# Kernel tuning notes

Hardware: AMD Instinct MI355X
Metric: run time of the kernel (lower is better)

Reference implementation:

```python
import jax, jax.numpy as jnp
import numpy as np

# Lorentz hyperboloid with curvature -1 (k = 1): <x,x>_L = -1/k, x0 = time coord.
K_CURV = 1.0
EPS = 1e-8
B, N, D, H = 4, 1024, 1024, 16
HD = D // H  # dim_per_head = 64 (space dims per head)


def _time(space):
    # time coord so the point lies on the hyperboloid
    return jnp.sqrt(jnp.sum(space * space, axis=-1, keepdims=True) + 1.0 / K_CURV)


def _lift(space):
    return jnp.concatenate([_time(space), space], axis=-1)


def _linner(u, v):
    # Minkowski inner product <u,v>_L = -u0 v0 + u_s . v_s
    return jnp.sum(u[..., 1:] * v[..., 1:], axis=-1) - u[..., 0] * v[..., 0]


def _lorentz_layernorm(x, gamma, beta):
    s = x[..., 1:]
    mu = jnp.mean(s, axis=-1, keepdims=True)
    var = jnp.mean((s - mu) ** 2, axis=-1, keepdims=True)
    s = (s - mu) / jnp.sqrt(var + 1e-5) * gamma + beta
    return _lift(s)


def _lorentz_linear(x, W, b):
    # linear on the full Lorentz point -> space part of output, time recomputed
    return _lift(x @ W + b)


def _lresnet(x, y, w):
    # Lorentzian residual: (x + w*y) renormalized back onto the hyperboloid
    z = x + w * y
    denom = jnp.sqrt(jnp.clip(-_linner(z, z), EPS))[..., None]
    return z / (jnp.sqrt(K_CURV) * denom)


def _attention(x, Wq, bq, Wk, bk, Wv, bv, Wo, bo):
    def heads(W, b):
        s = (x @ W + b).reshape(B, N, H, HD).transpose(0, 2, 1, 3)  # [B,H,N,HD]
        return _lift(s)  # per-head Lorentz points [B,H,N,HD+1]

    q, k, v = heads(Wq, bq), heads(Wk, bk), heads(Wv, bv)
    sgn = jnp.concatenate([-jnp.ones((1,), x.dtype), jnp.ones((HD,), x.dtype)])
    # pairwise Minkowski inner products; score = -d_L^2 = 2/k + 2<q,k>_L, scaled
    scores = jnp.einsum('bhqd,bhkd->bhqk', q * sgn, k)
    scores = (2.0 / K_CURV + 2.0 * scores) / np.sqrt(HD).astype(np.float32)
    attn = jax.nn.softmax(scores, axis=-1)
    # Lorentz midpoint aggregation of values
    mid = jnp.einsum('bhqk,bhkd->bhqd', attn, v)
    denom = jnp.sqrt(jnp.clip(-_linner(mid, mid), EPS))[..., None]
    mid = mid / (jnp.sqrt(K_CURV) * denom)  # [B,H,N,HD+1]
    cat = mid.transpose(0, 2, 1, 3).reshape(B, N, H * (HD + 1))  # trans_heads_concat
    return _lift(cat @ Wo + bo)


def reference(x, g1, b1, Wq, bq, Wk, bk, Wv, bv, Wo, bo, g2, b2, Wfc, bfc, Wpj, bpj, w1, w2):
    lx = _lorentz_layernorm(x, g1, b1)
    ax = _attention(lx, Wq, bq, Wk, bk, Wv, bv, Wo, bo)
    x = _lresnet(x, ax, w1)
    h = _lorentz_layernorm(x, g2, b2)
    h = _lorentz_linear(h, Wfc, bfc)                      # [B,N,4D]
    h = _lift(jax.nn.gelu(h[..., 1:], approximate=False))  # LorentzActivation(GELU)
    h = _lorentz_linear(h, Wpj, bpj)                      # [B,N,D]
    return _lresnet(x, h, w2)


def setup_inputs() -> dict:
    key = jax.random.key(0)
    ks = jax.random.split(key, 8)
    sc = 0.02
    f32 = jnp.float32
    xs = jax.random.normal(ks[0], (B, N, D - 1), f32)
    return dict(
        x=_lift(xs),
        g1=jnp.ones((D - 1,), f32), b1=jnp.zeros((D - 1,), f32),
        Wq=sc * jax.random.normal(ks[1], (D, H * HD), f32), bq=jnp.zeros((H * HD,), f32),
        Wk=sc * jax.random.normal(ks[2], (D, H * HD), f32), bk=jnp.zeros((H * HD,), f32),
        Wv=sc * jax.random.normal(ks[3], (D, H * HD), f32), bv=jnp.zeros((H * HD,), f32),
        Wo=sc * jax.random.normal(ks[4], (H * (HD + 1), D - 1), f32), bo=jnp.zeros((D - 1,), f32),
        g2=jnp.ones((D - 1,), f32), b2=jnp.zeros((D - 1,), f32),
        Wfc=sc * jax.random.normal(ks[5], (D, 4 * D - 1), f32), bfc=jnp.zeros((4 * D - 1,), f32),
        Wpj=sc * jax.random.normal(ks[6], (4 * D, D - 1), f32), bpj=jnp.zeros((D - 1,), f32),
        w1=jnp.ones((), f32), w2=jnp.ones((), f32),
    )
```

## Files before the change

### kernel.cpp

```cpp
#include <hip/hip_runtime.h>
#include <math.h>

#define BB 4
#define NN 1024
#define DD 1024
#define HH 16
#define ROWS (BB*NN)

typedef __attribute__((ext_vector_type(8))) short bf16x8;
typedef __attribute__((ext_vector_type(4))) float f32x4;
typedef unsigned short u16;

__device__ __forceinline__ u16 f2bf(float f) {
    union { float f; unsigned u; } v; v.f = f;
    unsigned r = v.u + 0x7fff + ((v.u >> 16) & 1);
    return (u16)(r >> 16);
}
__device__ __forceinline__ float bf2f(u16 u) {
    union { unsigned u; float f; } v; v.u = ((unsigned)u) << 16; return v.f;
}

__device__ __forceinline__ void async16(const void* g, void* l) {
    __builtin_amdgcn_global_load_lds(
        (__attribute__((address_space(1))) void*)(uintptr_t)g,
        (__attribute__((address_space(3))) void*)(uintptr_t)l,
        16, 0, 0);
}

__device__ __forceinline__ float block_reduce_sum(float v, float* sm) {
    #pragma unroll
    for (int o = 32; o > 0; o >>= 1) v += __shfl_down(v, o);
    int lane = threadIdx.x & 63, wid = threadIdx.x >> 6;
    if (lane == 0) sm[wid] = v;
    __syncthreads();
    if (wid == 0) {
        v = (lane < (int)(blockDim.x >> 6)) ? sm[lane] : 0.f;
        #pragma unroll
        for (int o = 2; o > 0; o >>= 1) v += __shfl_down(v, o);
        if (lane == 0) sm[0] = v;
    }
    __syncthreads();
    float r = sm[0];
    __syncthreads();
    return r;
}

__global__ __launch_bounds__(256) void k_pre(
        const float* __restrict__ Wq_, const float* __restrict__ Wk_,
        const float* __restrict__ Wv_, const float* __restrict__ Wo_,
        const float* __restrict__ Wfc_, const float* __restrict__ Wpj_,
        u16* __restrict__ WqkvT, u16* __restrict__ WoT,
        u16* __restrict__ WfcT, u16* __restrict__ WpjT,
        const float* __restrict__ x, const float* __restrict__ g1,
        const float* __restrict__ be1, u16* __restrict__ lnout) {
    __shared__ float t[32][33];
    int bid = blockIdx.x;
    if (bid < 12352) {
        const float* W; u16* out; int K, N, Kpad, Npad, gx;
        if (bid < 1024)      { W = Wq_;  out = WqkvT;            K = 1024; N = 1024; Kpad = 1024; Npad = 1024; gx = 32; }
        else if (bid < 2048) { W = Wk_;  out = WqkvT + 1048576;  K = 1024; N = 1024; Kpad = 1024; Npad = 1024; gx = 32; bid -= 1024; }
        else if (bid < 3072) { W = Wv_;  out = WqkvT + 2097152;  K = 1024; N = 1024; Kpad = 1024; Npad = 1024; gx = 32; bid -= 2048; }
        else if (bid < 4160) { W = Wo_;  out = WoT;              K = 1040; N = 1023; Kpad = 1088; Npad = 1024; gx = 34; bid -= 3072; }
        else if (bid < 8256) { W = Wfc_; out = WfcT;             K = 1024; N = 4095; Kpad = 1024; Npad = 4096; gx = 32; bid -= 4160; }
        else                 { W = Wpj_; out = WpjT;             K = 4096; N = 1023; Kpad = 4096; Npad = 1024; gx = 128; bid -= 8256; }
        int k0 = (bid % gx) * 32, n0 = (bid / gx) * 32;
        int tx = threadIdx.x & 31, ty = threadIdx.x >> 5;
        #pragma unroll
        for (int i = 0; i < 32; i += 8) {
            int k = k0 + ty + i, n = n0 + tx;
            t[ty + i][tx] = (k < K && n < N) ? W[(size_t)k * N + n] : 0.f;
        }
        __syncthreads();
        #pragma unroll
        for (int i = 0; i < 32; i += 8) {
            int n = n0 + ty + i, k = k0 + tx;
            if (n < Npad && k < Kpad) out[(size_t)n * Kpad + k] = f2bf(t[tx][ty + i]);
        }
    } else {
        float* sm = &t[0][0];
        int row = bid - 12352;
        const float* xr = x + (size_t)row * DD;
        u16* orow = lnout + (size_t)row * DD;
        float s = 0.f, ss = 0.f;
        for (int j = threadIdx.x; j < DD - 1; j += blockDim.x) {
            float v = xr[1 + j]; s += v; ss += v * v;
        }
        s = block_reduce_sum(s, sm);
        ss = block_reduce_sum(ss, sm);
        float mu = s / (float)(DD - 1);
        float var = ss / (float)(DD - 1) - mu * mu;
        float rstd = rsqrtf(var + 1e-5f);
        float s2 = 0.f;
        for (int j = threadIdx.x; j < DD - 1; j += blockDim.x) {
            float v = (xr[1 + j] - mu) * rstd * g1[j] + be1[j];
            orow[1 + j] = f2bf(v); s2 += v * v;
        }
        s2 = block_reduce_sum(s2, sm);
        if (threadIdx.x == 0) orow[0] = f2bf(sqrtf(s2 + 1.f));
    }
}

__device__ __forceinline__ void cstore(float* p, float v) { *p = v; }
__device__ __forceinline__ void cstore(u16* p, float v) { *p = f2bf(v); }

template <typename OT>
__global__ __launch_bounds__(256) void k_gemm_mfma(
        const u16* __restrict__ A, const u16* __restrict__ BT,
        const float* __restrict__ bias, int nbias,
        OT* __restrict__ C0, OT* __restrict__ C1,
        int ldc, int ldab, int ksplit, int K) {
    __shared__ __align__(16) u16 As[2][128 * 64];
    __shared__ __align__(16) u16 Bs[2][128 * 64];
    int z = blockIdx.z;
    int kbeg = z ? ksplit : 0;
    int kend = z ? K : ksplit;
    OT* C = z ? C1 : C0;
    const float* bs = z ? nullptr : bias;

    int tid = threadIdx.x;
    int wave = tid >> 6, lane = tid & 63;
    int quad = lane >> 4, m16 = lane & 15;
    int n0 = blockIdx.x * 128, m0 = blockIdx.y * 128;
    int wm = (wave & 1) * 64, wn = (wave >> 1) * 64;

    f32x4 acc[4][4];
    #pragma unroll
    for (int t = 0; t < 4; ++t)
        #pragma unroll
        for (int u = 0; u < 4; ++u) acc[t][u] = (f32x4){0.f, 0.f, 0.f, 0.f};

    int r8 = lane >> 3;
    int cc = (lane & 7) ^ r8;
    int srow = wave * 32 + r8;
    const u16* ag = A  + (size_t)(m0 + srow) * ldab + cc * 8;
    const u16* bg = BT + (size_t)(n0 + srow) * ldab + cc * 8;

    auto stage = [&](int k0, int s) {
        #pragma unroll
        for (int j = 0; j < 4; ++j) {
            async16(ag + (size_t)(j * 8) * ldab + k0, &As[s][(wave * 32 + j * 8) * 64]);
            async16(bg + (size_t)(j * 8) * ldab + k0, &Bs[s][(wave * 32 + j * 8) * 64]);
        }
    };

    int niter = (kend - kbeg) >> 6;
    stage(kbeg, 0);
    for (int it = 0; it < niter; ++it) {
        int cur = it & 1;
        __syncthreads();
        if (it + 1 < niter) stage(kbeg + (it + 1) * 64, cur ^ 1);
        #pragma unroll
        for (int kk = 0; kk < 2; ++kk) {
            bf16x8 af[4], bfr[4];
            #pragma unroll
            for (int t = 0; t < 4; ++t) {
                int slot = (kk * 4 + quad) ^ (m16 & 7);
                af[t] = *(const bf16x8*)&As[cur][(wm + t * 16 + m16) * 64 + slot * 8];
            }
            #pragma unroll
            for (int u = 0; u < 4; ++u) {
                int slot = (kk * 4 + quad) ^ (m16 & 7);
                bfr[u] = *(const bf16x8*)&Bs[cur][(wn + u * 16 + m16) * 64 + slot * 8];
            }
            #pragma unroll
            for (int t = 0; t < 4; ++t)
                #pragma unroll
                for (int u = 0; u < 4; ++u)
                    acc[t][u] = __builtin_amdgcn_mfma_f32_16x16x32_bf16(af[t], bfr[u], acc[t][u], 0, 0, 0);
        }
    }
    #pragma unroll
    for (int u = 0; u < 4; ++u) {
        int col = n0 + wn + u * 16 + m16;
        float bv = (bs != nullptr && col < nbias) ? bs[col] : 0.f;
        #pragma unroll
        for (int t = 0; t < 4; ++t) {
            #pragma unroll
            for (int r = 0; r < 4; ++r) {
                int row = m0 + wm + t * 16 + quad * 4 + r;
                cstore(C + (size_t)row * ldc + col, acc[t][u][r] + bv);
            }
        }
    }
}

__global__ __launch_bounds__(256) void k_build_heads(
        const u16* __restrict__ qkv,
        const float* __restrict__ bq, const float* __restrict__ bk,
        const float* __restrict__ bv,
        u16* __restrict__ Qp, u16* __restrict__ Kp, u16* __restrict__ V2) {
    int wid = threadIdx.x >> 6, lane = threadIdx.x & 63;
    int idx = blockIdx.x * 4 + wid;
    int h = idx & 15, bn = idx >> 4;
    int b = bn >> 10, n = bn & 1023;
    int sec = blockIdx.y;
    const float* bias = (sec == 0) ? bq : (sec == 1) ? bk : bv;
    float v = bf2f(qkv[(size_t)bn * 3072 + sec * 1024 + h * 64 + lane]) + bias[h * 64 + lane];
    float ss = v * v;
    #pragma unroll
    for (int o = 32; o > 0; o >>= 1) ss += __shfl_xor(ss, o);
    float tcomp = sqrtf(ss + 1.f);
    size_t bhn = (size_t)(b * 16 + h) * 1024 + n;
    if (sec == 0) {
        u16* drow = Qp + bhn * 96;
        drow[1 + lane] = f2bf(v);
        if (lane == 0) drow[0] = f2bf(-tcomp);
        if (lane < 31) drow[65 + lane] = 0;
    } else if (sec == 1) {
        u16* drow = Kp + bhn * 104;
        drow[1 + lane] = f2bf(v);
        if (lane == 0) drow[0] = f2bf(tcomp);
        if (lane < 39) drow[65 + lane] = 0;
    } else {
        u16* base = V2 + ((size_t)(b * 16 + h) * 16 + (n >> 6)) * 6144 + (n & 63);
        base[(1 + lane) * 72] = f2bf(v);
        if (lane == 0) base[0] = f2bf(tcomp);
        if (lane >= 49) base[(16 + lane) * 72] = 0;
    }
}

#define AKS 104
#define AVS 72
#define APS 88
#define KTILE_U16 (64 * AKS)
#define VTILE_U16 6144
#define EXPC 0.36067376f
__global__ __launch_bounds__(256) void k_attn_mfma(
        const u16* __restrict__ Qp, const u16* __restrict__ Kp,
        const u16* __restrict__ V2, u16* __restrict__ cat) {
    __shared__ __align__(16) u16 Klds[2][KTILE_U16];
    __shared__ __align__(16) u16 Vlds[2][VTILE_U16];
    __shared__ __align__(16) u16 Plds[4][16 * APS];
    int tid = threadIdx.x;
    int wave = tid >> 6, lane = tid & 63;
    int quad = lane >> 4, m = lane & 15;
    int bid = blockIdx.x;
    int bh = ((bid & 7) << 3) | (bid >> 6);
    int qt = (bid >> 3) & 7;

    const u16* kg = Kp + (size_t)bh * 16 * KTILE_U16;
    const u16* vg = V2 + (size_t)bh * 16 * VTILE_U16;

    bf16x8 aq[2][3];
    #pragma unroll
    for (int g = 0; g < 2; ++g) {
        const u16* qptr = Qp + ((size_t)bh * 1024 + qt * 128 + g * 64 + wave * 16 + m) * 96;
        aq[g][0] = *(const bf16x8*)(qptr + quad * 8);
        aq[g][1] = *(const bf16x8*)(qptr + 32 + quad * 8);
        aq[g][2] = *(const bf16x8*)(qptr + 64 + quad * 8);
    }

    f32x4 O[2][5];
    #pragma unroll
    for (int g = 0; g < 2; ++g)
        #pragma unroll
        for (int i = 0; i < 5; ++i) O[g][i] = (f32x4){0.f, 0.f, 0.f, 0.f};

    auto stage = [&](int kt, int s) {
        const u16* kt_p = kg + kt * KTILE_U16 + lane * 8;
        const u16* vt_p = vg + kt * VTILE_U16 + lane * 8;
        for (int i = wave; i < 25; i += 4) {
            if (i < 13) async16(kt_p + i * 512, &Klds[s][i * 512]);
            else        async16(vt_p + (i - 13) * 512, &Vlds[s][(i - 13) * 512]);
        }
    };

    stage(0, 0);
    for (int kt = 0; kt < 16; ++kt) {
        int cur = kt & 1;
        __syncthreads();
        if (kt < 15) stage(kt + 1, cur ^ 1);
        u16* pw = &Plds[wave][0];
        #pragma unroll
        for (int g = 0; g < 2; ++g) {
            #pragma unroll
            for (int nt = 0; nt < 4; ++nt) {
                f32x4 acc = (f32x4){0.f, 0.f, 0.f, 0.f};
                const u16* kr = &Klds[cur][(nt * 16 + m) * AKS + quad * 8];
                acc = __builtin_amdgcn_mfma_f32_16x16x32_bf16(*(const bf16x8*)(kr),      aq[g][0], acc, 0, 0, 0);
                acc = __builtin_amdgcn_mfma_f32_16x16x32_bf16(*(const bf16x8*)(kr + 32), aq[g][1], acc, 0, 0, 0);
                acc = __builtin_amdgcn_mfma_f32_16x16x32_bf16(*(const bf16x8*)(kr + 64), aq[g][2], acc, 0, 0, 0);
                unsigned pk0, pk1;
                {
                    union { float f; unsigned u; } a0, a1, a2, a3;
                    a0.f = __builtin_amdgcn_exp2f(fmaf(acc[0], EXPC, EXPC));
                    a1.f = __builtin_amdgcn_exp2f(fmaf(acc[1], EXPC, EXPC));
                    a2.f = __builtin_amdgcn_exp2f(fmaf(acc[2], EXPC, EXPC));
                    a3.f = __builtin_amdgcn_exp2f(fmaf(acc[3], EXPC, EXPC));
                    pk0 = ((a0.u + 0x8000u) >> 16) | (((a1.u + 0x8000u) >> 16) << 16);
                    pk1 = ((a2.u + 0x8000u) >> 16) | (((a3.u + 0x8000u) >> 16) << 16);
                }
                uint2 pk; pk.x = pk0; pk.y = pk1;
                *(uint2*)&pw[m * APS + nt * 16 + quad * 4] = pk;
            }
            #pragma unroll
            for (int kc = 0; kc < 2; ++kc) {
                bf16x8 ap = *(const bf16x8*)&Plds[wave][m * APS + kc * 32 + quad * 8];
                #pragma unroll
                for (int vt = 0; vt < 5; ++vt) {
                    bf16x8 bv = *(const bf16x8*)&Vlds[cur][(vt * 16 + m) * AVS + kc * 32 + quad * 8];
                    O[g][vt] = __builtin_amdgcn_mfma_f32_16x16x32_bf16(ap, bv, O[g][vt], 0, 0, 0);
                }
            }
        }
    }
    int b = bh >> 4, h = bh & 15;
    #pragma unroll
    for (int g = 0; g < 2; ++g) {
        #pragma unroll
        for (int r = 0; r < 4; ++r) {
            float part = 0.f;
            #pragma unroll
            for (int vt = 0; vt < 5; ++vt) {
                int c = vt * 16 + m;
                float o = O[g][vt][r];
                part += (c == 0) ? o * o : -o * o;
            }
            part += __shfl_xor(part, 1);
            part += __shfl_xor(part, 2);
            part += __shfl_xor(part, 4);
            part += __shfl_xor(part, 8);
            float rden = rsqrtf(fmaxf(part, 1e-8f));
            int n = qt * 128 + g * 64 + wave * 16 + quad * 4 + r;
            u16* crow = cat + (size_t)(b * 1024 + n) * 1088 + h * 65;
            #pragma unroll
            for (int vt = 0; vt < 5; ++vt) {
                int c = vt * 16 + m;
                if (c < 65) crow[c] = f2bf(O[g][vt][r] * rden);
            }
        }
    }
    if (h == 15) {
        for (int i = tid; i < 128 * 48; i += 256) {
            int rr = i / 48, c = i - rr * 48;
            int n = qt * 128 + rr;
            cat[(size_t)(b * 1024 + n) * 1088 + 1040 + c] = 0;
        }
    }
}

__global__ __launch_bounds__(256) void k_lresnet_ln(
        const float* __restrict__ x, const float* __restrict__ y0,
        const float* __restrict__ y1, const float* __restrict__ wscale,
        const float* __restrict__ g2, const float* __restrict__ be2,
        float* __restrict__ x1, u16* __restrict__ lnout) {
    __shared__ float sm[8];
    int row = blockIdx.x;
    const float* xr = x + (size_t)row * DD;
    const float* ya = y0 + (size_t)row * 1024;
    const float* yb = y1 + (size_t)row * 1024;
    float w = *wscale;
    float zreg[4];
    float sy = 0.f, sz = 0.f, szs = 0.f;
    int cnt = 0;
    for (int j = threadIdx.x; j < DD - 1; j += blockDim.x) {
        float yv = ya[j] + yb[j];
        float zv = xr[1 + j] + w * yv;
        sy += yv * yv; sz += zv * zv; szs += zv;
        zreg[cnt++] = zv;
    }
    sy = block_reduce_sum(sy, sm);
    sz = block_reduce_sum(sz, sm);
    szs = block_reduce_sum(szs, sm);
    float y0t = sqrtf(sy + 1.f);
    float z0 = xr[0] + w * y0t;
    float q = z0 * z0 - sz;
    float rden = rsqrtf(fmaxf(q, 1e-8f));
    float mu = rden * szs / (float)(DD - 1);
    float ex2 = rden * rden * sz / (float)(DD - 1);
    float var = ex2 - mu * mu;
    float rstd = rsqrtf(var + 1e-5f);
    float s2 = 0.f;
    cnt = 0;
    float* x1r = x1 + (size_t)row * DD;
    u16* lr = lnout + (size_t)row * DD;
    for (int j = threadIdx.x; j < DD - 1; j += blockDim.x) {
        float xv = zreg[cnt++] * rden;
        x1r[1 + j] = xv;
        float v = (xv - mu) * rstd * g2[j] + be2[j];
        lr[1 + j] = f2bf(v); s2 += v * v;
    }
    s2 = block_reduce_sum(s2, sm);
    if (threadIdx.x == 0) {
        x1r[0] = z0 * rden;
        lr[0] = f2bf(sqrtf(s2 + 1.f));
    }
}

__global__ __launch_bounds__(256) void k_lresnet(
        const float* __restrict__ x, const float* __restrict__ y0,
        const float* __restrict__ y1, const float* __restrict__ wscale,
        float* __restrict__ out) {
    __shared__ float sm[8];
    int row = blockIdx.x;
    const float* xr = x + (size_t)row * DD;
    const float* ya = y0 + (size_t)row * 1024;
    const float* yb = y1 + (size_t)row * 1024;
    float w = *wscale;
    float zreg[4];
    float sy = 0.f, sz = 0.f;
    int cnt = 0;
    for (int j = threadIdx.x; j < DD - 1; j += blockDim.x) {
        float yv = ya[j] + yb[j];
        float zv = xr[1 + j] + w * yv;
        sy += yv * yv; sz += zv * zv;
        zreg[cnt++] = zv;
    }
    sy = block_reduce_sum(sy, sm);
    sz = block_reduce_sum(sz, sm);
    float y0t = sqrtf(sy + 1.f);
    float z0 = xr[0] + w * y0t;
    float q = z0 * z0 - sz;
    float rden = rsqrtf(fmaxf(q, 1e-8f));
    cnt = 0;
    for (int j = threadIdx.x; j < DD - 1; j += blockDim.x)
        out[(size_t)row * DD + 1 + j] = zreg[cnt++] * rden;
    if (threadIdx.x == 0) out[(size_t)row * DD] = z0 * rden;
}

__global__ __launch_bounds__(256) void k_gelu_lift(
        const u16* __restrict__ hfc, u16* __restrict__ hg) {
    __shared__ float sm[8];
    int row = blockIdx.x;
    const u16* hr = hfc + (size_t)row * 4096;
    u16* gr = hg + (size_t)row * 4096;
    float s2 = 0.f;
    for (int j = threadIdx.x; j < 4095; j += blockDim.x) {
        float v = bf2f(hr[j]);
        float gl = 0.5f * v * (1.f + erff(v * 0.70710678f));
        gr[1 + j] = f2bf(gl); s2 += gl * gl;
    }
    s2 = block_reduce_sum(s2, sm);
    if (threadIdx.x == 0) gr[0] = f2bf(sqrtf(s2 + 1.f));
}

extern "C" void kernel_launch(void* const* d_in, const int* in_sizes, int n_in,
                              void* d_out, int out_size, void* d_ws, size_t ws_size,
                              hipStream_t stream) {
    const float* x   = (const float*)d_in[0];
    const float* g1  = (const float*)d_in[1];
    const float* b1  = (const float*)d_in[2];
    const float* Wq  = (const float*)d_in[3];
    const float* bq  = (const float*)d_in[4];
    const float* Wk  = (const float*)d_in[5];
    const float* bk  = (const float*)d_in[6];
    const float* Wv  = (const float*)d_in[7];
    const float* bv  = (const float*)d_in[8];
    const float* Wo  = (const float*)d_in[9];
    const float* bo  = (const float*)d_in[10];
    const float* g2  = (const float*)d_in[11];
    const float* b2  = (const float*)d_in[12];
    const float* Wfc = (const float*)d_in[13];
    const float* bfc = (const float*)d_in[14];
    const float* Wpj = (const float*)d_in[15];
    const float* bpj = (const float*)d_in[16];
    const float* w1  = (const float*)d_in[17];
    const float* w2  = (const float*)d_in[18];
    float* out = (float*)d_out;

    char* W = (char*)d_ws;
    u16* lx_bf  = (u16*)(W + 0);
    u16* WqkvT  = (u16*)(W + 8388608);
    u16* WoT    = (u16*)(W + 14680064);
    u16* WfcT   = (u16*)(W + 16908288);
    u16* WpjT   = (u16*)(W + 25296896);
    u16* qkv_bf = (u16*)(W + 33685504);
    u16* Qp     = (u16*)(W + 58851328);
    u16* Kp     = (u16*)(W + 71434240);
    u16* V2     = (u16*)(W + 85065728);
    u16* cat_bf = (u16*)(W + 97648640);
    float* ax0  = (float*)(W + 33685504);
    float* ax1  = (float*)(W + 50462720);
    float* x1   = (float*)(W + 67239936);
    u16* hfc_bf = (u16*)(W + 84017152);
    u16* hg_bf  = (u16*)(W + 33685504);
    float* h2a  = (float*)(W + 84017152);
    float* h2b  = (float*)(W + 100794368);

    dim3 blk(256);

    k_pre<<<16448, blk, 0, stream>>>(Wq, Wk, Wv, Wo, Wfc, Wpj,
                                     WqkvT, WoT, WfcT, WpjT,
                                     x, g1, b1, lx_bf);

    k_gemm_mfma<u16><<<dim3(24, 32, 1), blk, 0, stream>>>(
        lx_bf, WqkvT, nullptr, 0, qkv_bf, qkv_bf, 3072, 1024, 1024, 1024);
    k_build_heads<<<dim3(ROWS * HH / 4, 3), blk, 0, stream>>>(
        qkv_bf, bq, bk, bv, Qp, Kp, V2);

    k_attn_mfma<<<512, blk, 0, stream>>>(Qp, Kp, V2, cat_bf);

    k_gemm_mfma<float><<<dim3(8, 32, 2), blk, 0, stream>>>(
        cat_bf, WoT, bo, 1023, ax0, ax1, 1024, 1088, 576, 1088);

    k_lresnet_ln<<<ROWS, blk, 0, stream>>>(x, ax0, ax1, w1, g2, b2, x1, lx_bf);

    k_gemm_mfma<u16><<<dim3(32, 32, 1), blk, 0, stream>>>(
        lx_bf, WfcT, bfc, 4095, hfc_bf, hfc_bf, 4096, 1024, 1024, 1024);

    k_gelu_lift<<<ROWS, blk, 0, stream>>>(hfc_bf, hg_bf);

    k_gemm_mfma<float><<<dim3(8, 32, 2), blk, 0, stream>>>(
        hg_bf, WpjT, bpj, 1023, h2a, h2b, 1024, 4096, 2048, 4096);

    k_lresnet<<<ROWS, blk, 0, stream>>>(x1, h2a, h2b, w2, out);
}
```

Measured before the change: 441.1 us.

## Fuse QKV GEMM with per-head Lorentz lift and layout scatter

Replaces the QKV GEMM plus separate build-heads kernel with one GEMM whose epilogue adds bias, computes the per-head time coordinate via lane shuffles, and writes Q/K/V directly in the padded attention layouts. This removes the bf16 qkv intermediate round-trip and one kernel launch. In exchange the epilogue does scattered writes with extra shuffles and a heavier register load, which may affect the GEMM's efficiency.

```diff
diff --git a/kernel.cpp b/kernel.cpp
--- a/kernel.cpp
+++ b/kernel.cpp
@@ -9,6 +9,7 @@
 
 typedef __attribute__((ext_vector_type(8))) short bf16x8;
 typedef __attribute__((ext_vector_type(4))) float f32x4;
+typedef __attribute__((ext_vector_type(4))) unsigned short u16x4;
 typedef unsigned short u16;
 
 __device__ __forceinline__ u16 f2bf(float f) {
@@ -184,38 +185,126 @@
     }
 }
 
-__global__ __launch_bounds__(256) void k_build_heads(
-        const u16* __restrict__ qkv,
+__global__ __launch_bounds__(256) void k_gemm_qkv(
+        const u16* __restrict__ A, const u16* __restrict__ BT,
         const float* __restrict__ bq, const float* __restrict__ bk,
         const float* __restrict__ bv,
         u16* __restrict__ Qp, u16* __restrict__ Kp, u16* __restrict__ V2) {
-    int wid = threadIdx.x >> 6, lane = threadIdx.x & 63;
-    int idx = blockIdx.x * 4 + wid;
-    int h = idx & 15, bn = idx >> 4;
-    int b = bn >> 10, n = bn & 1023;
-    int sec = blockIdx.y;
+    __shared__ __align__(16) u16 As[2][128 * 64];
+    __shared__ __align__(16) u16 Bs[2][128 * 64];
+    int tid = threadIdx.x;
+    int wave = tid >> 6, lane = tid & 63;
+    int quad = lane >> 4, m16 = lane & 15;
+    int n0 = blockIdx.x * 128, m0 = blockIdx.y * 128;
+    int wm = (wave & 1) * 64, wn = (wave >> 1) * 64;
+
+    f32x4 acc[4][4];
+    #pragma unroll
+    for (int t = 0; t < 4; ++t)
+        #pragma unroll
+        for (int u = 0; u < 4; ++u) acc[t][u] = (f32x4){0.f, 0.f, 0.f, 0.f};
+
+    int r8 = lane >> 3;
+    int cc = (lane & 7) ^ r8;
+    int srow = wave * 32 + r8;
+    const u16* ag = A  + (size_t)(m0 + srow) * 1024 + cc * 8;
+    const u16* bg = BT + (size_t)(n0 + srow) * 1024 + cc * 8;
+
+    auto stage = [&](int k0, int s) {
+        #pragma unroll
+        for (int j = 0; j < 4; ++j) {
+            async16(ag + (size_t)(j * 8) * 1024 + k0, &As[s][(wave * 32 + j * 8) * 64]);
+            async16(bg + (size_t)(j * 8) * 1024 + k0, &Bs[s][(wave * 32 + j * 8) * 64]);
+        }
+    };
+
+    stage(0, 0);
+    for (int it = 0; it < 16; ++it) {
+        int cur = it & 1;
+        __syncthreads();
+        if (it + 1 < 16) stage((it + 1) * 64, cur ^ 1);
+        #pragma unroll
+        for (int kk = 0; kk < 2; ++kk) {
+            bf16x8 af[4], bfr[4];
+            #pragma unroll
+            for (int t = 0; t < 4; ++t) {
+                int slot = (kk * 4 + quad) ^ (m16 & 7);
+                af[t] = *(const bf16x8*)&As[cur][(wm + t * 16 + m16) * 64 + slot * 8];
+            }
+            #pragma unroll
+            for (int u = 0; u < 4; ++u) {
+                int slot = (kk * 4 + quad) ^ (m16 & 7);
+                bfr[u] = *(const bf16x8*)&Bs[cur][(wn + u * 16 + m16) * 64 + slot * 8];
+            }
+            #pragma unroll
+            for (int t = 0; t < 4; ++t)
+                #pragma unroll
+                for (int u = 0; u < 4; ++u)
+                    acc[t][u] = __builtin_amdgcn_mfma_f32_16x16x32_bf16(af[t], bfr[u], acc[t][u], 0, 0, 0);
+        }
+    }
+
+    int sec = n0 >> 10;
+    int h = ((n0 & 1023) + wn) >> 6;
+    int b = m0 >> 10;
+    int b16h = b * 16 + h;
     const float* bias = (sec == 0) ? bq : (sec == 1) ? bk : bv;
-    float v = bf2f(qkv[(size_t)bn * 3072 + sec * 1024 + h * 64 + lane]) + bias[h * 64 + lane];
-    float ss = v * v;
-    #pragma unroll
-    for (int o = 32; o > 0; o >>= 1) ss += __shfl_xor(ss, o);
-    float tcomp = sqrtf(ss + 1.f);
-    size_t bhn = (size_t)(b * 16 + h) * 1024 + n;
-    if (sec == 0) {
-        u16* drow = Qp + bhn * 96;
-        drow[1 + lane] = f2bf(v);
-        if (lane == 0) drow[0] = f2bf(-tcomp);
-        if (lane < 31) drow[65 + lane] = 0;
-    } else if (sec == 1) {
-        u16* drow = Kp + bhn * 104;
-        drow[1 + lane] = f2bf(v);
-        if (lane == 0) drow[0] = f2bf(tcomp);
-        if (lane < 39) drow[65 + lane] = 0;
+    float bvu[4];
+    #pragma unroll
+    for (int u = 0; u < 4; ++u) bvu[u] = bias[h * 64 + u * 16 + m16];
+
+    if (sec < 2) {
+        const int strd = (sec == 0) ? 96 : 104;
+        u16* P = (sec == 0) ? Qp : Kp;
+        const float tsign = (sec == 0) ? -1.f : 1.f;
+        #pragma unroll
+        for (int t = 0; t < 4; ++t) {
+            #pragma unroll
+            for (int r = 0; r < 4; ++r) {
+                int n = (m0 + wm + t * 16 + quad * 4 + r) & 1023;
+                u16* drow = P + ((size_t)b16h * 1024 + n) * strd;
+                float vv[4]; float ss = 0.f;
+                #pragma unroll
+                for (int u = 0; u < 4; ++u) { vv[u] = acc[t][u][r] + bvu[u]; ss += vv[u] * vv[u]; }
+                ss += __shfl_xor(ss, 1); ss += __shfl_xor(ss, 2);
+                ss += __shfl_xor(ss, 4); ss += __shfl_xor(ss, 8);
+                #pragma unroll
+                for (int u = 0; u < 4; ++u) drow[1 + u * 16 + m16] = f2bf(vv[u]);
+                if (m16 == 0) drow[0] = f2bf(tsign * sqrtf(ss + 1.f));
+                drow[65 + m16] = 0;
+                if (m16 < 15) drow[81 + m16] = 0;
+            }
+        }
     } else {
-        u16* base = V2 + ((size_t)(b * 16 + h) * 16 + (n >> 6)) * 6144 + (n & 63);
-        base[(1 + lane) * 72] = f2bf(v);
-        if (lane == 0) base[0] = f2bf(tcomp);
-        if (lane >= 49) base[(16 + lane) * 72] = 0;
+        int tile = ((m0 & 1023) + wm) >> 6;
+        size_t tbase = ((size_t)b16h * 16 + tile) * 6144;
+        #pragma unroll
+        for (int t = 0; t < 4; ++t) {
+            int tok0 = t * 16 + quad * 4;
+            u16x4 tc;
+            u16x4 pk[4];
+            #pragma unroll
+            for (int r = 0; r < 4; ++r) {
+                float vv[4]; float ss = 0.f;
+                #pragma unroll
+                for (int u = 0; u < 4; ++u) { vv[u] = acc[t][u][r] + bvu[u]; ss += vv[u] * vv[u]; }
+                ss += __shfl_xor(ss, 1); ss += __shfl_xor(ss, 2);
+                ss += __shfl_xor(ss, 4); ss += __shfl_xor(ss, 8);
+                tc[r] = f2bf(sqrtf(ss + 1.f));
+                #pragma unroll
+                for (int u = 0; u < 4; ++u) pk[u][r] = f2bf(vv[u]);
+            }
+            #pragma unroll
+            for (int u = 0; u < 4; ++u) {
+                int d = u * 16 + m16;
+                *(u16x4*)&V2[tbase + (size_t)(1 + d) * 72 + tok0] = pk[u];
+            }
+            if (m16 == 0) *(u16x4*)&V2[tbase + tok0] = tc;
+        }
+        for (int i = lane; i < 240; i += 64) {
+            int rr = 65 + (i >> 4), sg = (i & 15) << 2;
+            *(u16x4*)&V2[tbase + (size_t)rr * 72 + sg] = (u16x4){0, 0, 0, 0};
+        }
     }
 }
 
@@ -464,7 +553,6 @@
     u16* WoT    = (u16*)(W + 14680064);
     u16* WfcT   = (u16*)(W + 16908288);
     u16* WpjT   = (u16*)(W + 25296896);
-    u16* qkv_bf = (u16*)(W + 33685504);
     u16* Qp     = (u16*)(W + 58851328);
     u16* Kp     = (u16*)(W + 71434240);
     u16* V2     = (u16*)(W + 85065728);
@@ -483,10 +571,8 @@
                                      WqkvT, WoT, WfcT, WpjT,
                                      x, g1, b1, lx_bf);
 
-    k_gemm_mfma<u16><<<dim3(24, 32, 1), blk, 0, stream>>>(
-        lx_bf, WqkvT, nullptr, 0, qkv_bf, qkv_bf, 3072, 1024, 1024, 1024);
-    k_build_heads<<<dim3(ROWS * HH / 4, 3), blk, 0, stream>>>(
-        qkv_bf, bq, bk, bv, Qp, Kp, V2);
+    k_gemm_qkv<<<dim3(24, 32, 1), blk, 0, stream>>>(
+        lx_bf, WqkvT, bq, bk, bv, Qp, Kp, V2);
 
     k_attn_mfma<<<512, blk, 0, stream>>>(Qp, Kp, V2, cat_bf);
 
```

Result: faster. 406.1 us (-7.9%).
